# Optimization experiments

Hardware: AMD Instinct MI355X
Metric: run time of the kernel (lower is better)

The kernel has to match this reference:

```python
import jax, jax.numpy as jnp
import numpy as np

CHUNK = 2048  # query chunk for KNN to avoid materializing full [B,N,N] distances
BN_EPS = 1e-5


def knn_idx(xyz, k):
    """xyz: [B,N,3] -> idx [B,N,k] of k nearest points (incl. self), like keops argKmin."""
    B, N, _ = xyz.shape
    nc = N // CHUNK
    qs = jnp.moveaxis(xyz.reshape(B, nc, CHUNK, 3), 1, 0)  # [nc,B,CHUNK,3]

    def chunk_fn(q):  # q: [B,CHUNK,3]
        d = jnp.sum((q[:, :, None, :] - xyz[:, None, :, :]) ** 2, axis=-1)  # [B,CHUNK,N]
        _, idx = jax.lax.top_k(-d, k)
        return idx

    idx = jax.lax.map(chunk_fn, qs)  # [nc,B,CHUNK,k]
    return jnp.moveaxis(idx, 0, 1).reshape(B, N, k)


def setup_inputs() -> dict:
    key = jax.random.key(0)
    k1, k2, k3, k4 = jax.random.split(key, 4)
    B, N, C = 4, 16384, 128
    return {
        "xyz": jax.random.normal(k1, (B, N, 3), dtype=jnp.float32),
        "x": jax.random.normal(k2, (B, C, N), dtype=jnp.float32),
        "conv_w": jax.random.normal(k3, (C, C), dtype=jnp.float32) * (1.0 / np.sqrt(C)),
        "conv_b": jax.random.normal(k4, (C,), dtype=jnp.float32) * 0.01,
        "gamma": jnp.ones((C,), dtype=jnp.float32),
        "beta": jnp.zeros((C,), dtype=jnp.float32),
        "k": 16,
    }


def reference(xyz, x, conv_w, conv_b, gamma, beta, k):
    # KNN on coordinates
    idx = knn_idx(xyz, k)                       # [B,N,k]
    xt = jnp.swapaxes(x, 1, 2)                  # [B,N,C]
    neigh = jax.vmap(lambda p, i: p[i])(xt, idx)  # [B,N,k,C] gather per batch
    # dx = sum over k neighbors minus center feature (Laplacian-like)
    dx = jnp.swapaxes(neigh.sum(axis=2) - xt, 1, 2)  # [B,C,N]
    # conv1x1 -> relu -> batchnorm (training-mode batch stats) -> residual
    h = jax.nn.relu(jnp.einsum('oc,bcn->bon', conv_w, dx) + conv_b[None, :, None])
    mean = h.mean(axis=(0, 2))
    var = h.var(axis=(0, 2))  # biased variance, as torch BN normalization
    hn = (h - mean[None, :, None]) * jax.lax.rsqrt(var[None, :, None] + BN_EPS)
    return x + gamma[None, :, None] * hn + beta[None, :, None]
```

## Files before the change

kernel.cpp:

```cpp
#include <hip/hip_runtime.h>

#define BATCH 4
#define NPTS  16384
#define CH    128
#define KNN   16

#define G      64
#define GRID3  (G * G * G)
#define GW     0.25f
#define GINVW  4.0f
#define GORIG  (-8.0f)
#define OCCW   (GRID3 / 32)

#define XT_OFF    0
#define HT_OFF    33554432
#define CNT_OFF   33554432
#define CUR_OFF   37748736
#define HDR_OFF   41943040
#define OCC_OFF   50331648
#define SPTS_OFF  50462720
#define GCTR_OFF  51511296
#define IDX_OFF   67108864
#define PART_OFF  71303168
#define STATS_OFF 75497472

__device__ __forceinline__ int cell1(float v) {
    int c = (int)floorf((v - GORIG) * GINVW);
    return min(G - 1, max(0, c));
}

__global__ __launch_bounds__(256) void zero_kernel(int* __restrict__ p, int n,
                                                   int* __restrict__ gctr) {
    int i = blockIdx.x * 256 + threadIdx.x;
    if (i < BATCH) gctr[i] = 0;
    const int stride = gridDim.x * 256;
    for (; i < n; i += stride) p[i] = 0;
}

__global__ __launch_bounds__(256) void transpose_kernel(const float* __restrict__ x,
                                                        float* __restrict__ xt) {
    __shared__ float t[32][33];
    const int b  = blockIdx.z;
    const int c0 = blockIdx.y * 32;
    const int n0 = blockIdx.x * 32;
    const int tx = threadIdx.x, ty = threadIdx.y;
#pragma unroll
    for (int i = 0; i < 4; ++i)
        t[ty + 8 * i][tx] = x[((size_t)b * CH + c0 + ty + 8 * i) * NPTS + n0 + tx];
    __syncthreads();
#pragma unroll
    for (int i = 0; i < 4; ++i)
        xt[((size_t)b * NPTS + n0 + ty + 8 * i) * CH + c0 + tx] = t[tx][ty + 8 * i];
}

__global__ __launch_bounds__(256) void count_kernel(const float* __restrict__ xyz,
                                                    int* __restrict__ counts) {
    const int b = blockIdx.y;
    const int i = blockIdx.x * 256 + threadIdx.x;
    const float* p = xyz + ((size_t)b * NPTS + i) * 3;
    const int c = (cell1(p[2]) * G + cell1(p[1])) * G + cell1(p[0]);
    atomicAdd(&counts[(size_t)b * GRID3 + c], 1);
}

__global__ __launch_bounds__(256) void cellhdr_kernel(const int* __restrict__ counts,
                                                      int2* __restrict__ hdr,
                                                      unsigned int* __restrict__ occ,
                                                      int* __restrict__ gctr) {
    const int cid  = blockIdx.x * 256 + threadIdx.x;
    const int b    = cid >> 18;
    const int lane = threadIdx.x & 63;
    const int c    = counts[cid];

    int incl = c;
#pragma unroll
    for (int off = 1; off < 64; off <<= 1) {
        int t = __shfl_up(incl, off);
        if (lane >= off) incl += t;
    }
    const int excl = incl - c;
    const int tot  = __shfl(incl, 63);

    const unsigned long long ball = __ballot(c > 0);
    if (lane == 0) {
        const int w = cid >> 5;
        occ[w]     = (unsigned int)ball;
        occ[w + 1] = (unsigned int)(ball >> 32);
    }

    int base = 0;
    if (lane == 63) base = atomicAdd(&gctr[b], tot);
    base = __shfl(base, 63);

    if (c > 0) hdr[cid] = make_int2(base + excl, c);
}

__global__ __launch_bounds__(256) void scatter_kernel(const float* __restrict__ xyz,
                                                      const int2* __restrict__ hdr,
                                                      int* __restrict__ cursor,
                                                      float4* __restrict__ spts) {
    const int b = blockIdx.y;
    const int i = blockIdx.x * 256 + threadIdx.x;
    const float* p = xyz + ((size_t)b * NPTS + i) * 3;
    const float x = p[0], y = p[1], z = p[2];
    const int c = (cell1(z) * G + cell1(y)) * G + cell1(x);
    const int pos = hdr[(size_t)b * GRID3 + c].x + atomicAdd(&cursor[(size_t)b * GRID3 + c], 1);
    spts[(size_t)b * NPTS + pos] = make_float4(x, y, z, __int_as_float(i));
}

__global__ __launch_bounds__(256) void knn_grid_kernel(const float4* __restrict__ spts,
                                                       const int2* __restrict__ hdr,
                                                       const unsigned int* __restrict__ occ,
                                                       int* __restrict__ idx_out) {
    __shared__ unsigned int socc[OCCW];
    const int b   = blockIdx.y;
    const int tid = threadIdx.x;
    for (int i = tid; i < OCCW; i += 256) socc[i] = occ[(size_t)b * OCCW + i];
    __syncthreads();

    const int s = blockIdx.x * 256 + tid;
    const float4 P = spts[(size_t)b * NPTS + s];
    const float qx = P.x, qy = P.y, qz = P.z;
    const int qi = __float_as_int(P.w);
    const int cx = cell1(qx), cy = cell1(qy), cz = cell1(qz);
    const int2* hb = hdr + (size_t)b * GRID3;
    const float4* pts = spts + (size_t)b * NPTS;

    float dq[KNN]; int iq[KNN];
#pragma unroll
    for (int t = 0; t < KNN; ++t) { dq[t] = 3.0e38f; iq[t] = 0x7fffffff; }

    for (int R = 0; R < G; ++R) {
        if (R > 0) {
            const int rm = R - 1;
            float dmin = 3.0e38f;
            bool any = false;
            if (cx - rm > 0)     { dmin = fminf(dmin, qx - (GORIG + (cx - rm) * GW)); any = true; }
            if (cx + rm < G - 1) { dmin = fminf(dmin, (GORIG + (cx + rm + 1) * GW) - qx); any = true; }
            if (cy - rm > 0)     { dmin = fminf(dmin, qy - (GORIG + (cy - rm) * GW)); any = true; }
            if (cy + rm < G - 1) { dmin = fminf(dmin, (GORIG + (cy + rm + 1) * GW) - qy); any = true; }
            if (cz - rm > 0)     { dmin = fminf(dmin, qz - (GORIG + (cz - rm) * GW)); any = true; }
            if (cz + rm < G - 1) { dmin = fminf(dmin, (GORIG + (cz + rm + 1) * GW) - qz); any = true; }
            if (!any) break;
            dmin = fmaxf(dmin, 0.0f);
            if (dq[KNN - 1] < dmin * dmin * (1.0f - 1e-5f)) break;
        }
        const int z0 = max(0, cz - R), z1 = min(G - 1, cz + R);
        const int y0 = max(0, cy - R), y1 = min(G - 1, cy + R);
        const int x0 = max(0, cx - R), x1 = min(G - 1, cx + R);
        for (int z = z0; z <= z1; ++z) {
            const int az = (z > cz) ? (z - cz) : (cz - z);
            const float lz = GORIG + z * GW;
            const float dzc = fmaxf(fmaxf(lz - qz, qz - (lz + GW)), 0.0f);
            for (int y = y0; y <= y1; ++y) {
                const int ay = (y > cy) ? (y - cy) : (cy - y);
                const float ly = GORIG + y * GW;
                const float dyc = fmaxf(fmaxf(ly - qy, qy - (ly + GW)), 0.0f);
                const float dzy = dzc * dzc + dyc * dyc;
                const int row = z * G + y;

                unsigned long long m;
                if (az == R || ay == R) {
                    m = (~0ull >> (63 - (x1 - x0))) << x0;
                } else {
                    m = 0ull;
                    if (cx - R >= 0) m |= 1ull << (cx - R);
                    if (cx + R < G)  m |= 1ull << (cx + R);
                }
                m &= (unsigned long long)socc[row * 2] |
                     ((unsigned long long)socc[row * 2 + 1] << 32);

                while (m) {
                    const int x = __ffsll(m) - 1;
                    m &= m - 1;
                    const float lx = GORIG + x * GW;
                    const float dxc = fmaxf(fmaxf(lx - qx, qx - (lx + GW)), 0.0f);
                    const float cmin = dzy + dxc * dxc;
                    if (cmin * (1.0f - 1e-5f) > dq[KNN - 1]) continue;
                    const int2 hc = hb[row * G + x];
                    const int en = hc.x + hc.y;
                    for (int j = hc.x; j < en; ++j) {
                        const float4 pp = pts[j];
                        const float ddx = __fsub_rn(qx, pp.x);
                        const float ddy = __fsub_rn(qy, pp.y);
                        const float ddz = __fsub_rn(qz, pp.z);
                        const float d = __fadd_rn(__fadd_rn(__fmul_rn(ddx, ddx), __fmul_rn(ddy, ddy)),
                                                  __fmul_rn(ddz, ddz));
                        const int oi = __float_as_int(pp.w);
                        if (d < dq[KNN - 1] || (d == dq[KNN - 1] && oi < iq[KNN - 1])) {
                            float cd = d; int ci = oi;
#pragma unroll
                            for (int t2 = KNN - 1; t2 >= 1; --t2) {
                                const bool lt = (cd < dq[t2 - 1]) ||
                                                (cd == dq[t2 - 1] && ci < iq[t2 - 1]);
                                if (lt) {
                                    dq[t2] = dq[t2 - 1]; iq[t2] = iq[t2 - 1];
                                    if (t2 == 1) { dq[0] = cd; iq[0] = ci; }
                                } else {
                                    dq[t2] = cd; iq[t2] = ci;
                                    break;
                                }
                            }
                        }
                    }
                }
            }
        }
    }

    int* op = idx_out + ((size_t)b * NPTS + qi) * KNN;
#pragma unroll
    for (int t = 0; t < KNN; ++t) op[t] = iq[t];
}

__global__ __launch_bounds__(128) void conv_kernel(const float* __restrict__ xt,
                                                   const int* __restrict__ idx,
                                                   const float* __restrict__ W,
                                                   const float* __restrict__ bias,
                                                   float* __restrict__ h_t,
                                                   float* __restrict__ partials) {
    __shared__ __align__(16) float dxbuf[CH];
    const int o   = threadIdx.x;
    const int blk = blockIdx.x;
    const int b   = blk / (NPTS / 16);
    const int n0  = (blk % (NPTS / 16)) * 16;

    float4 w4[CH / 4];
    const float4* wrow = (const float4*)(W + (size_t)o * CH);
#pragma unroll
    for (int i = 0; i < CH / 4; ++i) w4[i] = wrow[i];
    const float bo = bias[o];

    const float* xb = xt + (size_t)b * NPTS * CH;
    float sS = 0.0f, sQ = 0.0f;

    for (int r = 0; r < 16; ++r) {
        const int n = n0 + r;
        const int* ip = idx + ((size_t)b * NPTS + n) * KNN;
        int jj[KNN];
#pragma unroll
        for (int k = 0; k < KNN; ++k) jj[k] = ip[k];
        float va[KNN];
#pragma unroll
        for (int k = 0; k < KNN; ++k) va[k] = xb[(size_t)jj[k] * CH + o];
        const float ctr = xb[(size_t)n * CH + o];
        float acc = 0.0f;
#pragma unroll
        for (int k = 0; k < KNN; ++k) acc += va[k];
        acc -= ctr;

        dxbuf[o] = acc;
        __syncthreads();

        float h = bo;
        const float4* d4 = (const float4*)dxbuf;
#pragma unroll
        for (int cc = 0; cc < CH / 4; ++cc) {
            const float4 a = d4[cc];
            const float4 w = w4[cc];
            h = fmaf(w.x, a.x, h);
            h = fmaf(w.y, a.y, h);
            h = fmaf(w.z, a.z, h);
            h = fmaf(w.w, a.w, h);
        }
        h = fmaxf(h, 0.0f);
        h_t[((size_t)b * NPTS + n) * CH + o] = h;
        sS += h;
        sQ += h * h;
        __syncthreads();
    }

    partials[(size_t)o * 4096 + blk]        = sS;
    partials[(size_t)(CH + o) * 4096 + blk] = sQ;
}

__global__ __launch_bounds__(256) void bnred_kernel(const float* __restrict__ partials,
                                                    float* __restrict__ stats) {
    const int ch = blockIdx.x;
    const float* pS = partials + (size_t)ch * 4096;
    const float* pQ = partials + (size_t)(CH + ch) * 4096;
    float s = 0.0f, q = 0.0f;
    for (int i = threadIdx.x; i < 4096; i += 256) { s += pS[i]; q += pQ[i]; }
#pragma unroll
    for (int off = 32; off > 0; off >>= 1) {
        s += __shfl_down(s, off);
        q += __shfl_down(q, off);
    }
    __shared__ float wsum[4][2];
    const int wid = threadIdx.x >> 6;
    if ((threadIdx.x & 63) == 0) { wsum[wid][0] = s; wsum[wid][1] = q; }
    __syncthreads();
    if (threadIdx.x == 0) {
        const float S = wsum[0][0] + wsum[1][0] + wsum[2][0] + wsum[3][0];
        const float Q = wsum[0][1] + wsum[1][1] + wsum[2][1] + wsum[3][1];
        const float inv  = 1.0f / (float)(BATCH * NPTS);
        const float mean = S * inv;
        const float var  = Q * inv - mean * mean;
        stats[ch]      = mean;
        stats[CH + ch] = rsqrtf(var + 1e-5f);
    }
}

__global__ __launch_bounds__(256) void final_kernel(const float* __restrict__ x,
                                                    const float* __restrict__ h_t,
                                                    const float* __restrict__ stats,
                                                    const float* __restrict__ gamma,
                                                    const float* __restrict__ beta,
                                                    float* __restrict__ out) {
    __shared__ float t[32][33];
    const int b  = blockIdx.z;
    const int o0 = blockIdx.y * 32;
    const int n0 = blockIdx.x * 32;
    const int tx = threadIdx.x, ty = threadIdx.y;
#pragma unroll
    for (int i = 0; i < 4; ++i)
        t[ty + 8 * i][tx] = h_t[((size_t)b * NPTS + n0 + ty + 8 * i) * CH + o0 + tx];
    __syncthreads();
#pragma unroll
    for (int i = 0; i < 4; ++i) {
        const int o = o0 + ty + 8 * i;
        const float mean = stats[o];
        const float rstd = stats[CH + o];
        const float g = gamma[o], be = beta[o];
        const size_t offp = ((size_t)b * CH + o) * NPTS + n0 + tx;
        out[offp] = x[offp] + g * ((t[tx][ty + 8 * i] - mean) * rstd) + be;
    }
}

extern "C" void kernel_launch(void* const* d_in, const int* in_sizes, int n_in,
                              void* d_out, int out_size, void* d_ws, size_t ws_size,
                              hipStream_t stream) {
    const float* xyz    = (const float*)d_in[0];
    const float* x      = (const float*)d_in[1];
    const float* conv_w = (const float*)d_in[2];
    const float* conv_b = (const float*)d_in[3];
    const float* gamma  = (const float*)d_in[4];
    const float* beta   = (const float*)d_in[5];
    float* out = (float*)d_out;

    char* ws = (char*)d_ws;
    float*        xt     = (float*)(ws + XT_OFF);
    int*          counts = (int*)  (ws + CNT_OFF);
    int*          cursor = (int*)  (ws + CUR_OFF);
    int2*         hdr    = (int2*) (ws + HDR_OFF);
    unsigned int* occ    = (unsigned int*)(ws + OCC_OFF);
    float4*       spts   = (float4*)(ws + SPTS_OFF);
    int*          gctr   = (int*)  (ws + GCTR_OFF);
    float*        h_t    = (float*)(ws + HT_OFF);
    int*          idx    = (int*)  (ws + IDX_OFF);
    float*        part   = (float*)(ws + PART_OFF);
    float*        stats  = (float*)(ws + STATS_OFF);

    transpose_kernel<<<dim3(NPTS / 32, CH / 32, BATCH), dim3(32, 8), 0, stream>>>(x, xt);

    zero_kernel<<<dim3(2048), dim3(256), 0, stream>>>(counts, 2 * BATCH * GRID3, gctr);
    count_kernel<<<dim3(NPTS / 256, BATCH), dim3(256), 0, stream>>>(xyz, counts);
    cellhdr_kernel<<<dim3(BATCH * GRID3 / 256), dim3(256), 0, stream>>>(counts, hdr, occ, gctr);
    scatter_kernel<<<dim3(NPTS / 256, BATCH), dim3(256), 0, stream>>>(xyz, hdr, cursor, spts);

    knn_grid_kernel<<<dim3(NPTS / 256, BATCH), dim3(256), 0, stream>>>(spts, hdr, occ, idx);

    conv_kernel<<<dim3(BATCH * NPTS / 16), dim3(128), 0, stream>>>(xt, idx, conv_w, conv_b, h_t, part);
    bnred_kernel<<<dim3(CH), dim3(256), 0, stream>>>(part, stats);
    final_kernel<<<dim3(NPTS / 32, CH / 32, BATCH), dim3(32, 8), 0, stream>>>(x, h_t, stats, gamma, beta, out);
}
```

Baseline: 804.3 us.

## Rewrite KNN as wave-per-query search with cooperative candidate buffering

```diff
diff --git a/kernel.cpp b/kernel.cpp
--- a/kernel.cpp
+++ b/kernel.cpp
@@ -11,6 +11,9 @@
 #define GINVW  4.0f
 #define GORIG  (-8.0f)
 #define OCCW   (GRID3 / 32)
+
+#define QWAVES 1024
+#define QPW    (NPTS / QWAVES)
 
 #define XT_OFF    0
 #define HT_OFF    33554432
@@ -29,6 +32,29 @@
     return min(G - 1, max(0, c));
 }
 
+__device__ __forceinline__ float axdist(float q, int c) {
+    const float lo = GORIG + c * GW;
+    return fmaxf(fmaxf(lo - q, q - (lo + GW)), 0.0f);
+}
+
+__device__ __forceinline__ bool lexlt(float d1, int i1, float d2, int i2) {
+    return (d1 < d2) || (d1 == d2 && i1 < i2);
+}
+
+__device__ __forceinline__ void insert_lex(float (&dq)[KNN], int (&iq)[KNN], float d, int oi) {
+    float cd = d; int ci = oi;
+#pragma unroll
+    for (int t = KNN - 1; t >= 1; --t) {
+        if (lexlt(cd, ci, dq[t - 1], iq[t - 1])) {
+            dq[t] = dq[t - 1]; iq[t] = iq[t - 1];
+            if (t == 1) { dq[0] = cd; iq[0] = ci; }
+        } else {
+            dq[t] = cd; iq[t] = ci;
+            break;
+        }
+    }
+}
+
 __global__ __launch_bounds__(256) void zero_kernel(int* __restrict__ p, int n,
                                                    int* __restrict__ gctr) {
     int i = blockIdx.x * 256 + threadIdx.x;
@@ -59,7 +85,7 @@
     const int i = blockIdx.x * 256 + threadIdx.x;
     const float* p = xyz + ((size_t)b * NPTS + i) * 3;
     const int c = (cell1(p[2]) * G + cell1(p[1])) * G + cell1(p[0]);
-    atomicAdd(&counts[(size_t)b * GRID3 + c], 1);
+    atomicAdd(&counts[((size_t)b << 18) + c], 1);
 }
 
 __global__ __launch_bounds__(256) void cellhdr_kernel(const int* __restrict__ counts,
@@ -103,113 +129,188 @@
     const float* p = xyz + ((size_t)b * NPTS + i) * 3;
     const float x = p[0], y = p[1], z = p[2];
     const int c = (cell1(z) * G + cell1(y)) * G + cell1(x);
-    const int pos = hdr[(size_t)b * GRID3 + c].x + atomicAdd(&cursor[(size_t)b * GRID3 + c], 1);
+    const int pos = hdr[((size_t)b << 18) + c].x + atomicAdd(&cursor[((size_t)b << 18) + c], 1);
     spts[(size_t)b * NPTS + pos] = make_float4(x, y, z, __int_as_float(i));
 }
 
-__global__ __launch_bounds__(256) void knn_grid_kernel(const float4* __restrict__ spts,
+__global__ __launch_bounds__(256) void knn_wave_kernel(const float4* __restrict__ spts,
                                                        const int2* __restrict__ hdr,
                                                        const unsigned int* __restrict__ occ,
                                                        int* __restrict__ idx_out) {
     __shared__ unsigned int socc[OCCW];
+    __shared__ float4 cbuf[4][64];
     const int b   = blockIdx.y;
     const int tid = threadIdx.x;
     for (int i = tid; i < OCCW; i += 256) socc[i] = occ[(size_t)b * OCCW + i];
     __syncthreads();
 
-    const int s = blockIdx.x * 256 + tid;
-    const float4 P = spts[(size_t)b * NPTS + s];
-    const float qx = P.x, qy = P.y, qz = P.z;
-    const int qi = __float_as_int(P.w);
-    const int cx = cell1(qx), cy = cell1(qy), cz = cell1(qz);
-    const int2* hb = hdr + (size_t)b * GRID3;
+    const int widx = tid >> 6;
+    const int lane = tid & 63;
+    const int wid  = blockIdx.x * 4 + widx;
+    const int2* hb = hdr + ((size_t)b << 18);
     const float4* pts = spts + (size_t)b * NPTS;
-
-    float dq[KNN]; int iq[KNN];
-#pragma unroll
-    for (int t = 0; t < KNN; ++t) { dq[t] = 3.0e38f; iq[t] = 0x7fffffff; }
-
-    for (int R = 0; R < G; ++R) {
-        if (R > 0) {
-            const int rm = R - 1;
-            float dmin = 3.0e38f;
-            bool any = false;
-            if (cx - rm > 0)     { dmin = fminf(dmin, qx - (GORIG + (cx - rm) * GW)); any = true; }
-            if (cx + rm < G - 1) { dmin = fminf(dmin, (GORIG + (cx + rm + 1) * GW) - qx); any = true; }
-            if (cy - rm > 0)     { dmin = fminf(dmin, qy - (GORIG + (cy - rm) * GW)); any = true; }
-            if (cy + rm < G - 1) { dmin = fminf(dmin, (GORIG + (cy + rm + 1) * GW) - qy); any = true; }
-            if (cz - rm > 0)     { dmin = fminf(dmin, qz - (GORIG + (cz - rm) * GW)); any = true; }
-            if (cz + rm < G - 1) { dmin = fminf(dmin, (GORIG + (cz + rm + 1) * GW) - qz); any = true; }
-            if (!any) break;
-            dmin = fmaxf(dmin, 0.0f);
-            if (dq[KNN - 1] < dmin * dmin * (1.0f - 1e-5f)) break;
-        }
-        const int z0 = max(0, cz - R), z1 = min(G - 1, cz + R);
-        const int y0 = max(0, cy - R), y1 = min(G - 1, cy + R);
-        const int x0 = max(0, cx - R), x1 = min(G - 1, cx + R);
-        for (int z = z0; z <= z1; ++z) {
-            const int az = (z > cz) ? (z - cz) : (cz - z);
-            const float lz = GORIG + z * GW;
-            const float dzc = fmaxf(fmaxf(lz - qz, qz - (lz + GW)), 0.0f);
-            for (int y = y0; y <= y1; ++y) {
-                const int ay = (y > cy) ? (y - cy) : (cy - y);
-                const float ly = GORIG + y * GW;
-                const float dyc = fmaxf(fmaxf(ly - qy, qy - (ly + GW)), 0.0f);
-                const float dzy = dzc * dzc + dyc * dyc;
-                const int row = z * G + y;
-
-                unsigned long long m;
-                if (az == R || ay == R) {
-                    m = (~0ull >> (63 - (x1 - x0))) << x0;
-                } else {
-                    m = 0ull;
-                    if (cx - R >= 0) m |= 1ull << (cx - R);
-                    if (cx + R < G)  m |= 1ull << (cx + R);
+    float4* cb = cbuf[widx];
+
+    for (int q = 0; q < QPW; ++q) {
+        const int s = wid + q * QWAVES;
+        const float4 P = pts[s];
+        const float qx = P.x, qy = P.y, qz = P.z;
+        const int qi = __float_as_int(P.w);
+        const int cx = cell1(qx), cy = cell1(qy), cz = cell1(qz);
+
+        float dq[KNN]; int iq[KNN];
+
+        const int w0 = s & ~63;
+        {
+            const float4 pp = pts[w0 + lane];
+            float d;
+            {
+                const float ddx = __fsub_rn(qx, pp.x);
+                const float ddy = __fsub_rn(qy, pp.y);
+                const float ddz = __fsub_rn(qz, pp.z);
+                d = __fadd_rn(__fadd_rn(__fmul_rn(ddx, ddx), __fmul_rn(ddy, ddy)),
+                              __fmul_rn(ddz, ddz));
+            }
+            int oi = __float_as_int(pp.w);
+#pragma unroll
+            for (int k = 2; k <= 64; k <<= 1) {
+#pragma unroll
+                for (int j = k >> 1; j >= 1; j >>= 1) {
+                    const float od = __shfl_xor(d, j);
+                    const int  ooi = __shfl_xor(oi, j);
+                    const bool wantMin = (((lane & j) == 0) == ((lane & k) == 0));
+                    const bool take = wantMin ? lexlt(od, ooi, d, oi)
+                                              : lexlt(d, oi, od, ooi);
+                    if (take) { d = od; oi = ooi; }
                 }
-                m &= (unsigned long long)socc[row * 2] |
-                     ((unsigned long long)socc[row * 2 + 1] << 32);
-
-                while (m) {
-                    const int x = __ffsll(m) - 1;
-                    m &= m - 1;
-                    const float lx = GORIG + x * GW;
-                    const float dxc = fmaxf(fmaxf(lx - qx, qx - (lx + GW)), 0.0f);
-                    const float cmin = dzy + dxc * dxc;
-                    if (cmin * (1.0f - 1e-5f) > dq[KNN - 1]) continue;
-                    const int2 hc = hb[row * G + x];
-                    const int en = hc.x + hc.y;
-                    for (int j = hc.x; j < en; ++j) {
-                        const float4 pp = pts[j];
-                        const float ddx = __fsub_rn(qx, pp.x);
-                        const float ddy = __fsub_rn(qy, pp.y);
-                        const float ddz = __fsub_rn(qz, pp.z);
-                        const float d = __fadd_rn(__fadd_rn(__fmul_rn(ddx, ddx), __fmul_rn(ddy, ddy)),
-                                                  __fmul_rn(ddz, ddz));
-                        const int oi = __float_as_int(pp.w);
-                        if (d < dq[KNN - 1] || (d == dq[KNN - 1] && oi < iq[KNN - 1])) {
-                            float cd = d; int ci = oi;
-#pragma unroll
-                            for (int t2 = KNN - 1; t2 >= 1; --t2) {
-                                const bool lt = (cd < dq[t2 - 1]) ||
-                                                (cd == dq[t2 - 1] && ci < iq[t2 - 1]);
-                                if (lt) {
-                                    dq[t2] = dq[t2 - 1]; iq[t2] = iq[t2 - 1];
-                                    if (t2 == 1) { dq[0] = cd; iq[0] = ci; }
-                                } else {
-                                    dq[t2] = cd; iq[t2] = ci;
-                                    break;
-                                }
-                            }
-                        }
+            }
+#pragma unroll
+            for (int t = 0; t < KNN; ++t) {
+                dq[t] = __shfl(d, t);
+                iq[t] = __shfl(oi, t);
+            }
+        }
+
+        int cnum = 0;
+
+        auto flushp = [&]() {
+            if (cnum == 0) return;
+            float d = 3.0e38f; int oi = 0x7fffffff;
+            if (lane < cnum) {
+                const float4 pp = cb[lane];
+                const float ddx = __fsub_rn(qx, pp.x);
+                const float ddy = __fsub_rn(qy, pp.y);
+                const float ddz = __fsub_rn(qz, pp.z);
+                d = __fadd_rn(__fadd_rn(__fmul_rn(ddx, ddx), __fmul_rn(ddy, ddy)),
+                              __fmul_rn(ddz, ddz));
+                oi = __float_as_int(pp.w);
+            }
+            for (int it = 0; it < KNN; ++it) {
+                float md = d; int mi = oi; int ml = lane;
+#pragma unroll
+                for (int off = 1; off < 64; off <<= 1) {
+                    const float od = __shfl_xor(md, off);
+                    const int  omi = __shfl_xor(mi, off);
+                    const int  oml = __shfl_xor(ml, off);
+                    if (lexlt(od, omi, md, mi)) { md = od; mi = omi; ml = oml; }
+                }
+                if (!lexlt(md, mi, dq[KNN - 1], iq[KNN - 1])) break;
+                insert_lex(dq, iq, md, mi);
+                if (lane == ml) { d = 3.0e38f; oi = 0x7fffffff; }
+            }
+            cnum = 0;
+        };
+
+        auto append = [&](int st, int en) {
+#pragma unroll
+            for (int part = 0; part < 2; ++part) {
+                int a = part ? max(st, w0 + 64) : st;
+                int e = part ? en : min(en, w0);
+                int c = e - a;
+                while (c > 0) {
+                    const int t = min(c, 64 - cnum);
+                    if (lane < t) cb[cnum + lane] = pts[a + lane];
+                    c -= t; a += t; cnum += t;
+                    if (cnum == 64) flushp();
+                }
+            }
+        };
+
+        {
+            const int2 hc = hb[(cz * G + cy) * G + cx];
+            append(hc.x, hc.x + hc.y);
+        }
+        flushp();
+
+        for (int R = 1; R < G; ++R) {
+            {
+                const int rm = R - 1;
+                float dmin = 3.0e38f;
+                bool any = false;
+                if (cx - rm > 0)     { dmin = fminf(dmin, qx - (GORIG + (cx - rm) * GW)); any = true; }
+                if (cx + rm < G - 1) { dmin = fminf(dmin, (GORIG + (cx + rm + 1) * GW) - qx); any = true; }
+                if (cy - rm > 0)     { dmin = fminf(dmin, qy - (GORIG + (cy - rm) * GW)); any = true; }
+                if (cy + rm < G - 1) { dmin = fminf(dmin, (GORIG + (cy + rm + 1) * GW) - qy); any = true; }
+                if (cz - rm > 0)     { dmin = fminf(dmin, qz - (GORIG + (cz - rm) * GW)); any = true; }
+                if (cz + rm < G - 1) { dmin = fminf(dmin, (GORIG + (cz + rm + 1) * GW) - qz); any = true; }
+                if (!any) break;
+                dmin = fmaxf(dmin, 0.0f);
+                if (dq[KNN - 1] < dmin * dmin * (1.0f - 1e-5f)) break;
+            }
+            const int z0 = max(0, cz - R), z1 = min(G - 1, cz + R);
+            const int y0 = max(0, cy - R), y1 = min(G - 1, cy + R);
+            const int x0 = max(0, cx - R), x1 = min(G - 1, cx + R);
+            const unsigned long long xm_full = (~0ull >> (63 - (x1 - x0))) << x0;
+
+            for (int z = z0; z <= z1; ++z) {
+                const int az = (z > cz) ? (z - cz) : (cz - z);
+                const float dzc = axdist(qz, z);
+                const float dz2 = dzc * dzc;
+                if (dz2 * (1.0f - 1e-5f) > dq[KNN - 1]) continue;
+                for (int y = y0; y <= y1; ++y) {
+                    const int ay = (y > cy) ? (y - cy) : (cy - y);
+                    const float dyc = axdist(qy, y);
+                    const float dzy = dz2 + dyc * dyc;
+                    if (dzy * (1.0f - 1e-5f) > dq[KNN - 1]) continue;
+                    const int row = z * G + y;
+
+                    unsigned long long m;
+                    if (az == R || ay == R) {
+                        m = xm_full;
+                    } else {
+                        m = 0ull;
+                        if (cx - R >= 0) m |= 1ull << (cx - R);
+                        if (cx + R < G)  m |= 1ull << (cx + R);
+                    }
+                    m &= (unsigned long long)socc[row * 2] |
+                         ((unsigned long long)socc[row * 2 + 1] << 32);
+
+                    while (m) {
+                        const int x = __ffsll(m) - 1;
+                        m &= m - 1;
+                        const float dxc = axdist(qx, x);
+                        const float cmin = dzy + dxc * dxc;
+                        if (cmin * (1.0f - 1e-5f) > dq[KNN - 1]) continue;
+                        const int2 hc = hb[row * G + x];
+                        append(hc.x, hc.x + hc.y);
                     }
                 }
             }
-        }
-    }
-
-    int* op = idx_out + ((size_t)b * NPTS + qi) * KNN;
-#pragma unroll
-    for (int t = 0; t < KNN; ++t) op[t] = iq[t];
+            flushp();
+        }
+
+        if (lane == 0) {
+            int* op = idx_out + ((size_t)b * NPTS + qi) * KNN;
+            int4 v0 = make_int4(iq[0], iq[1], iq[2], iq[3]);
+            int4 v1 = make_int4(iq[4], iq[5], iq[6], iq[7]);
+            int4 v2 = make_int4(iq[8], iq[9], iq[10], iq[11]);
+            int4 v3 = make_int4(iq[12], iq[13], iq[14], iq[15]);
+            ((int4*)op)[0] = v0;
+            ((int4*)op)[1] = v1;
+            ((int4*)op)[2] = v2;
+            ((int4*)op)[3] = v3;
+        }
+    }
 }
 
 __global__ __launch_bounds__(128) void conv_kernel(const float* __restrict__ xt,
@@ -357,7 +458,7 @@
     cellhdr_kernel<<<dim3(BATCH * GRID3 / 256), dim3(256), 0, stream>>>(counts, hdr, occ, gctr);
     scatter_kernel<<<dim3(NPTS / 256, BATCH), dim3(256), 0, stream>>>(xyz, hdr, cursor, spts);
 
-    knn_grid_kernel<<<dim3(NPTS / 256, BATCH), dim3(256), 0, stream>>>(spts, hdr, occ, idx);
+    knn_wave_kernel<<<dim3(QWAVES / 4, BATCH), dim3(256), 0, stream>>>(spts, hdr, occ, idx);
 
     conv_kernel<<<dim3(BATCH * NPTS / 16), dim3(128), 0, stream>>>(xt, idx, conv_w, conv_b, h_t, part);
     bnred_kernel<<<dim3(CH), dim3(256), 0, stream>>>(part, stats);
```

Result: slower. 1.588 ms (+97.4%).
